# Performance work log

Hardware: AMD Instinct MI355X
Metric: run time of the kernel (lower is better)

## Reference

```python
import jax, jax.numpy as jnp
import numpy as np

N_NODES = 100000
N_EDGES = 1600000
IN_C, HID_C, OUT_C = 64, 64, 40


def setup_inputs() -> dict:
    key = jax.random.key(0)
    ks = jax.random.split(key, 8)
    x = jax.random.normal(ks[0], (N_NODES, IN_C), dtype=jnp.float32)
    edge_index = jax.random.randint(ks[1], (2, N_EDGES), 0, N_NODES, dtype=jnp.int32)
    s = 1.0 / np.sqrt(HID_C)
    W1 = jax.random.uniform(ks[2], (IN_C, HID_C), jnp.float32, -s, s)
    b1 = jnp.zeros((HID_C,), jnp.float32)
    Wh = jax.random.uniform(ks[3], (HID_C, HID_C), jnp.float32, -s, s)
    bh = jnp.zeros((HID_C,), jnp.float32)
    W2 = jax.random.uniform(ks[4], (HID_C, OUT_C), jnp.float32, -s, s)
    b2 = jnp.zeros((OUT_C,), jnp.float32)
    return {"x": x, "edge_index": edge_index, "W1": W1, "b1": b1,
            "Wh": Wh, "bh": bh, "W2": W2, "b2": b2}


def reference(x, edge_index, W1, b1, Wh, bh, W2, b2):
    N = x.shape[0]
    loop = jnp.arange(N, dtype=edge_index.dtype)
    # GCN normalization with self-loops: A_hat = D^-1/2 (A + I) D^-1/2
    src = jnp.concatenate([edge_index[0], loop])  # [E + N]
    dst = jnp.concatenate([edge_index[1], loop])
    deg = jax.ops.segment_sum(jnp.ones_like(dst, dtype=x.dtype), dst, num_segments=N)
    dinv = jnp.where(deg > 0, jax.lax.rsqrt(deg), 0.0)
    norm = dinv[src] * dinv[dst]  # [E + N]

    def gcn_conv(h, W, b):
        h = h @ W                              # [N, out]
        msg = h[src] * norm[:, None]           # gather + scale, [E+N, out]
        return jax.ops.segment_sum(msg, dst, num_segments=N) + b

    h = jax.nn.relu(gcn_conv(x, W1, b1))       # conv1 (dropout = identity in eval)
    h = jax.nn.relu(gcn_conv(h, Wh, bh))       # hidden_conv, layer_size=2 -> one pass
    h = gcn_conv(h, W2, b2)                    # conv2
    return jax.nn.log_softmax(h, axis=1)
```

## Files before the change

kernel.cpp:

```cpp
#include <hip/hip_runtime.h>
#include <hip/hip_bf16.h>
#include <math.h>

#define EPT 16
#define BCAP 16384

typedef _Float16 half8 __attribute__((ext_vector_type(8)));
typedef _Float16 half2v __attribute__((ext_vector_type(2)));
typedef float f32x4 __attribute__((ext_vector_type(4)));

__device__ __forceinline__ unsigned short f16r(float f) {
    _Float16 h = (_Float16)f;
    return __builtin_bit_cast(unsigned short, h);
}
__device__ __forceinline__ half2v h2(unsigned u) {
    return __builtin_bit_cast(half2v, u);
}


__global__ void scat1_kernel(const int* __restrict__ src, const int* __restrict__ dst,
                             int* __restrict__ cntg, unsigned* __restrict__ ebuf, int E) {
    __shared__ int lh[256];
    __shared__ int lbase[256];
    int tid = threadIdx.x;
    lh[tid] = 0;
    __syncthreads();
    int base = blockIdx.x * (256 * EPT);
    int ds[EPT], ss[EPT];
#pragma unroll
    for (int k = 0; k < EPT; ++k) {
        int e = base + k * 256 + tid;
        ds[k] = (e < E) ? dst[e] : -1;
        ss[k] = (e < E) ? src[e] : 0;
    }
#pragma unroll
    for (int k = 0; k < EPT; ++k) {
        if (ds[k] >= 0) atomicAdd(&lh[ds[k] >> 9], 1);
    }
    __syncthreads();
    if (lh[tid] > 0) lbase[tid] = atomicAdd(&cntg[tid], lh[tid]);
    lh[tid] = 0;
    __syncthreads();
#pragma unroll
    for (int k = 0; k < EPT; ++k) {
        if (ds[k] >= 0) {
            int b = ds[k] >> 9;
            int pos = lbase[b] + atomicAdd(&lh[b], 1);
            ebuf[(size_t)b * BCAP + pos] = ((unsigned)ss[k] << 9) | (unsigned)(ds[k] & 511);
        }
    }
}

__global__ void build_kernel(const unsigned* __restrict__ ebuf, const int* __restrict__ cntg,
                             int* __restrict__ row_ptr, int* __restrict__ col,
                             float* __restrict__ dinv, int N, int E) {
    __shared__ int deg[512];
    __shared__ int sh[256];
    int b = blockIdx.x;
    int tid = threadIdx.x;

    int v = cntg[tid];
    sh[tid] = v;
    __syncthreads();
    int val = v;
    for (int off = 1; off < 256; off <<= 1) {
        int add = 0;
        if (tid >= off) add = sh[tid - off];
        __syncthreads();
        val += add;
        sh[tid] = val;
        __syncthreads();
    }
    int start = (b > 0) ? sh[b - 1] : 0;
    int cnt = cntg[b];
    __syncthreads();

    int nodeBase = b << 9;
    int nn = N - nodeBase;
    if (nn > 512) nn = 512;
    if (nn < 0) nn = 0;
    const unsigned* eb = ebuf + (size_t)b * BCAP;

    deg[tid] = 0;
    deg[tid + 256] = 0;
    __syncthreads();
    for (int j = tid; j < cnt; j += 256) {
        atomicAdd(&deg[eb[j] & 511u], 1);
    }
    __syncthreads();

    int i0 = tid * 2, i1 = i0 + 1;
    int v0 = deg[i0], v1 = deg[i1];
    int tot = v0 + v1;
    sh[tid] = tot;
    __syncthreads();
    int val2 = tot;
    for (int off = 1; off < 256; off <<= 1) {
        int add = 0;
        if (tid >= off) add = sh[tid - off];
        __syncthreads();
        val2 += add;
        sh[tid] = val2;
        __syncthreads();
    }
    int excl = val2 - tot;

    if (i0 < nn) { row_ptr[nodeBase + i0] = start + excl;      dinv[nodeBase + i0] = rsqrtf((float)v0 + 1.0f); }
    if (i1 < nn) { row_ptr[nodeBase + i1] = start + excl + v0; dinv[nodeBase + i1] = rsqrtf((float)v1 + 1.0f); }
    if (b == 0 && tid == 0) row_ptr[N] = E;
    deg[i0] = start + excl;
    deg[i1] = start + excl + v0;
    __syncthreads();

    for (int j = tid; j < cnt; j += 256) {
        unsigned rec = eb[j];
        int pos = atomicAdd(&deg[rec & 511u], 1);
        col[pos] = (int)(rec >> 9);
    }
}


__global__ void cvtpack_kernel(const float* __restrict__ x, unsigned short* __restrict__ xb,
                               int n4, int npad, const float* __restrict__ dinv,
                               const float* __restrict__ W1, const float* __restrict__ Wh,
                               const float* __restrict__ W2, unsigned short* __restrict__ wp1,
                               unsigned short* __restrict__ wph, unsigned short* __restrict__ wp2) {
    int bid = blockIdx.x;
    if (bid < 16) {
        int i = bid * 256 + threadIdx.x;
        int j = i & 7;
        int lane = (i >> 3) & 63;
        int hh = (i >> 9) & 1;
        int t = i >> 10;
        int k = hh * 32 + (lane >> 4) * 8 + j;
        int cc = t * 16 + (lane & 15);
        wp1[i] = f16r(W1[k * 64 + cc]);
        wph[i] = f16r(Wh[k * 64 + cc]);
        if (t < 3) wp2[i] = f16r(cc < 40 ? W2[k * 40 + cc] : 0.f);
    } else {
        if (bid == 16 && threadIdx.x < 8) {
            *(uint4*)(xb + (size_t)npad * 64 + threadIdx.x * 8) = make_uint4(0, 0, 0, 0);
        }
        int i = (bid - 16) * 256 + threadIdx.x;
        if (i < n4) {
            float dn = dinv[i >> 4];
            float4 v = *(const float4*)(x + (size_t)i * 4);
            ushort4 o;
            o.x = f16r(v.x * dn); o.y = f16r(v.y * dn);
            o.z = f16r(v.z * dn); o.w = f16r(v.w * dn);
            *(ushort4*)(xb + (size_t)i * 4) = o;
        }
    }
}


__launch_bounds__(256, 8)
__global__ void fused_relu_kernel(const unsigned short* __restrict__ h,
                                  const int* __restrict__ row_ptr,
                                  const int* __restrict__ col,
                                  const float* __restrict__ dinv,
                                  const unsigned short* __restrict__ wp,
                                  const float* __restrict__ bias,
                                  unsigned short* __restrict__ out,
                                  int n, int zrow) {
    __shared__ unsigned short tile[16][72];
    if (blockIdx.x == 0 && threadIdx.x < 8) {
        *(uint4*)(out + (size_t)zrow * 64 + threadIdx.x * 8) = make_uint4(0, 0, 0, 0);
    }
    int tid = threadIdx.x;
    int w = tid >> 6;
    int lane = tid & 63;
    int sub = lane >> 3;
    unsigned choff = (lane & 7) * 16u;
    int nodeBase = blockIdx.x * 16;

#pragma unroll 1
    for (int i = 0; i < 4; ++i) {
        int row = w * 4 + i;
        int node = nodeBase + row;
        half2v a0 = (half2v)0, a1 = (half2v)0, a2 = (half2v)0, a3 = (half2v)0;
        if (node < n) {
            int beg = row_ptr[node];
            int deg = row_ptr[node + 1] - beg;
            float di = dinv[node];
            int total = deg + 1;
            int base = 0;
            while (base < total) {
                int vi = base + lane;
                int idx = zrow;
                if (vi < deg) idx = col[beg + vi];
                else if (vi == deg) idx = node;
                int cnt = min(total - base, 64);
#pragma unroll
                for (int it = 0; it < 4; ++it) {
                    int c0 = it * 16;
                    if (c0 >= cnt) break;
                    int s0 = __shfl(idx, c0 + sub);
                    int s1 = __shfl(idx, c0 + 8 + sub);
                    uint4 u0 = *(const uint4*)((const char*)h + (((unsigned)s0 << 7) + choff));
                    uint4 u1 = *(const uint4*)((const char*)h + (((unsigned)s1 << 7) + choff));
                    a0 += h2(u0.x);  a1 += h2(u0.y);  a2 += h2(u0.z);  a3 += h2(u0.w);
                    a0 += h2(u1.x);  a1 += h2(u1.y);  a2 += h2(u1.z);  a3 += h2(u1.w);
                }
                base += cnt;
            }
#pragma unroll
            for (int off = 8; off <= 32; off <<= 1) {
                a0 += __builtin_bit_cast(half2v, __shfl_xor(__builtin_bit_cast(int, a0), off));
                a1 += __builtin_bit_cast(half2v, __shfl_xor(__builtin_bit_cast(int, a1), off));
                a2 += __builtin_bit_cast(half2v, __shfl_xor(__builtin_bit_cast(int, a2), off));
                a3 += __builtin_bit_cast(half2v, __shfl_xor(__builtin_bit_cast(int, a3), off));
            }
            if (sub == 0) {
                half2v dih = __builtin_bit_cast(half2v, __builtin_amdgcn_cvt_pkrtz(di, di));
                a0 *= dih; a1 *= dih; a2 *= dih; a3 *= dih;
                uint4 o;
                o.x = __builtin_bit_cast(unsigned, a0);
                o.y = __builtin_bit_cast(unsigned, a1);
                o.z = __builtin_bit_cast(unsigned, a2);
                o.w = __builtin_bit_cast(unsigned, a3);
                *(uint4*)((char*)&tile[row][0] + choff) = o;
            }
        } else if (sub == 0) {
            *(uint4*)((char*)&tile[row][0] + choff) = make_uint4(0, 0, 0, 0);
        }
    }
    __syncthreads();

    int q = lane >> 4, c = lane & 15;
    half8 bf0 = *(const half8*)(wp + w * 1024 + lane * 8);
    half8 bf1 = *(const half8*)(wp + w * 1024 + 512 + lane * 8);
    float bs = bias[w * 16 + c];
    half8 a0 = *(const half8*)&tile[c][q * 8];
    half8 a1 = *(const half8*)&tile[c][32 + q * 8];
    f32x4 z = {0.f, 0.f, 0.f, 0.f};
    z = __builtin_amdgcn_mfma_f32_16x16x32_f16(a0, bf0, z, 0, 0, 0);
    z = __builtin_amdgcn_mfma_f32_16x16x32_f16(a1, bf1, z, 0, 0, 0);
#pragma unroll
    for (int r = 0; r < 4; ++r) {
        int node = nodeBase + q * 4 + r;
        if (node < n) {
            float dn = dinv[node];
            out[(size_t)node * 64 + w * 16 + c] = f16r(fmaxf(z[r] + bs, 0.f) * dn);
        }
    }
}


__launch_bounds__(256, 8)
__global__ void fused_lsm_kernel(const unsigned short* __restrict__ h,
                                 const int* __restrict__ row_ptr,
                                 const int* __restrict__ col,
                                 const float* __restrict__ dinv,
                                 const unsigned short* __restrict__ wp,
                                 const float* __restrict__ bias,
                                 float* __restrict__ out,
                                 int n, int zrow) {
    __shared__ unsigned short tile[16][72];
    int tid = threadIdx.x;
    int w = tid >> 6;
    int lane = tid & 63;
    int sub = lane >> 3;
    unsigned choff = (lane & 7) * 16u;
    int nodeBase = blockIdx.x * 16;

#pragma unroll 1
    for (int i = 0; i < 4; ++i) {
        int row = w * 4 + i;
        int node = nodeBase + row;
        half2v a0 = (half2v)0, a1 = (half2v)0, a2 = (half2v)0, a3 = (half2v)0;
        if (node < n) {
            int beg = row_ptr[node];
            int deg = row_ptr[node + 1] - beg;
            float di = dinv[node];
            int total = deg + 1;
            int base = 0;
            while (base < total) {
                int vi = base + lane;
                int idx = zrow;
                if (vi < deg) idx = col[beg + vi];
                else if (vi == deg) idx = node;
                int cnt = min(total - base, 64);
#pragma unroll
                for (int it = 0; it < 4; ++it) {
                    int c0 = it * 16;
                    if (c0 >= cnt) break;
                    int s0 = __shfl(idx, c0 + sub);
                    int s1 = __shfl(idx, c0 + 8 + sub);
                    uint4 u0 = *(const uint4*)((const char*)h + (((unsigned)s0 << 7) + choff));
                    uint4 u1 = *(const uint4*)((const char*)h + (((unsigned)s1 << 7) + choff));
                    a0 += h2(u0.x);  a1 += h2(u0.y);  a2 += h2(u0.z);  a3 += h2(u0.w);
                    a0 += h2(u1.x);  a1 += h2(u1.y);  a2 += h2(u1.z);  a3 += h2(u1.w);
                }
                base += cnt;
            }
#pragma unroll
            for (int off = 8; off <= 32; off <<= 1) {
                a0 += __builtin_bit_cast(half2v, __shfl_xor(__builtin_bit_cast(int, a0), off));
                a1 += __builtin_bit_cast(half2v, __shfl_xor(__builtin_bit_cast(int, a1), off));
                a2 += __builtin_bit_cast(half2v, __shfl_xor(__builtin_bit_cast(int, a2), off));
                a3 += __builtin_bit_cast(half2v, __shfl_xor(__builtin_bit_cast(int, a3), off));
            }
            if (sub == 0) {
                half2v dih = __builtin_bit_cast(half2v, __builtin_amdgcn_cvt_pkrtz(di, di));
                a0 *= dih; a1 *= dih; a2 *= dih; a3 *= dih;
                uint4 o;
                o.x = __builtin_bit_cast(unsigned, a0);
                o.y = __builtin_bit_cast(unsigned, a1);
                o.z = __builtin_bit_cast(unsigned, a2);
                o.w = __builtin_bit_cast(unsigned, a3);
                *(uint4*)((char*)&tile[row][0] + choff) = o;
            }
        } else if (sub == 0) {
            *(uint4*)((char*)&tile[row][0] + choff) = make_uint4(0, 0, 0, 0);
        }
    }
    __syncthreads();
    if (w != 0) return;

    int q = lane >> 4, c = lane & 15;
    bool v2ok = (c < 8);

    half8 bfrag[3][2];
#pragma unroll
    for (int t = 0; t < 3; ++t)
#pragma unroll
        for (int hh = 0; hh < 2; ++hh)
            bfrag[t][hh] = *(const half8*)(wp + t * 1024 + hh * 512 + lane * 8);
    float bs[3];
    bs[0] = bias[c];
    bs[1] = bias[16 + c];
    bs[2] = v2ok ? bias[32 + c] : 0.f;

    half8 a0 = *(const half8*)&tile[c][q * 8];
    half8 a1 = *(const half8*)&tile[c][32 + q * 8];

    f32x4 acc[3];
#pragma unroll
    for (int t = 0; t < 3; ++t) {
        f32x4 z = {0.f, 0.f, 0.f, 0.f};
        z = __builtin_amdgcn_mfma_f32_16x16x32_f16(a0, bfrag[t][0], z, 0, 0, 0);
        z = __builtin_amdgcn_mfma_f32_16x16x32_f16(a1, bfrag[t][1], z, 0, 0, 0);
        acc[t] = z;
    }

#pragma unroll
    for (int r = 0; r < 4; ++r) {
        int node = nodeBase + q * 4 + r;
        if (node < n) {
            float v0 = acc[0][r] + bs[0];
            float v1 = acc[1][r] + bs[1];
            float v2 = v2ok ? (acc[2][r] + bs[2]) : -INFINITY;
            float m = fmaxf(fmaxf(v0, v1), v2);
#pragma unroll
            for (int off = 1; off <= 8; off <<= 1) m = fmaxf(m, __shfl_xor(m, off));
            float s = expf(v0 - m) + expf(v1 - m) + (v2ok ? expf(v2 - m) : 0.f);
#pragma unroll
            for (int off = 1; off <= 8; off <<= 1) s += __shfl_xor(s, off);
            float ls = m + logf(s);
            float* orow = out + (size_t)node * 40;
            orow[c] = v0 - ls;
            orow[16 + c] = v1 - ls;
            if (v2ok) orow[32 + c] = v2 - ls;
        }
    }
}


extern "C" void kernel_launch(void* const* d_in, const int* in_sizes, int n_in,
                              void* d_out, int out_size, void* d_ws, size_t ws_size,
                              hipStream_t stream) {
    const float* x  = (const float*)d_in[0];
    const int* ei   = (const int*)d_in[1];
    const float* W1 = (const float*)d_in[2];
    const float* b1 = (const float*)d_in[3];
    const float* Wh = (const float*)d_in[4];
    const float* bh = (const float*)d_in[5];
    const float* W2 = (const float*)d_in[6];
    const float* b2 = (const float*)d_in[7];
    float* out = (float*)d_out;

    const int N = in_sizes[0] / 64;
    const int E = in_sizes[1] / 2;
    const int nbuk = (N + 511) >> 9;
    const int nTiles = (N + 15) / 16;
    const int Npad = nTiles * 16;

    const int* srcp = ei;
    const int* dstp = ei + E;

    size_t off = 0;
    auto alloc = [&](size_t bytes) {
        size_t o = off;
        off = (off + bytes + 255) & ~(size_t)255;
        return o;
    };
    char* ws = (char*)d_ws;
    int*      cntg    = (int*)(ws + alloc(256 * 4));
    int*      row_ptr = (int*)(ws + alloc((size_t)(N + 1) * 4));
    float*    dinv    = (float*)(ws + alloc((size_t)N * 4));
    int*      col     = (int*)(ws + alloc((size_t)E * 4));
    unsigned* ebuf    = (unsigned*)(ws + alloc((size_t)nbuk * BCAP * 4));
    unsigned short* wp1  = (unsigned short*)(ws + alloc(4096 * 2));
    unsigned short* wph  = (unsigned short*)(ws + alloc(4096 * 2));
    unsigned short* wp2  = (unsigned short*)(ws + alloc(3072 * 2));
    unsigned short* xb   = (unsigned short*)(ws + alloc((size_t)(Npad + 1) * 64 * 2));
    unsigned short* gA   = (unsigned short*)(ws + alloc((size_t)(Npad + 1) * 64 * 2));
    unsigned short* gB   = (unsigned short*)(ws + alloc((size_t)(Npad + 1) * 64 * 2));
    (void)ws_size;

    hipMemsetAsync(cntg, 0, 256 * 4, stream);

    const int ebGrid = (E + 256 * EPT - 1) / (256 * EPT);
    scat1_kernel<<<ebGrid, 256, 0, stream>>>(srcp, dstp, cntg, ebuf, E);
    build_kernel<<<nbuk, 256, 0, stream>>>(ebuf, cntg, row_ptr, col, dinv, N, E);

    const int n4 = N * 16;
    cvtpack_kernel<<<16 + (n4 + 255) / 256, 256, 0, stream>>>(x, xb, n4, Npad, dinv,
                                                              W1, Wh, W2, wp1, wph, wp2);

    fused_relu_kernel<<<nTiles, 256, 0, stream>>>(xb, row_ptr, col, dinv, wp1, b1, gA, N, Npad);
    fused_relu_kernel<<<nTiles, 256, 0, stream>>>(gA, row_ptr, col, dinv, wph, bh, gB, N, Npad);
    fused_lsm_kernel<<<nTiles, 256, 0, stream>>>(gB, row_ptr, col, dinv, wp2, b2, out, N, Npad);
}
```

Measured before the change: 252.0 us.

## Aggregate four nodes per wavefront with 16-lane groups in fused GCN kernels

The neighbor-gather phase of both fused kernels now assigns one 16-lane group per node, so a wavefront handles its four destination rows concurrently rather than serially. Each group loops in 16-edge chunks up to the wave's maximum chunk count, using two interleaved half-precision accumulator sets to shorten dependency chains. The cross-lane reduction shrinks to one shuffle step. This targets underutilised lanes and serial latency for low-degree nodes, at the cost of intra-wave imbalance when the four node degrees differ.

```diff
diff --git a/kernel.cpp b/kernel.cpp
--- a/kernel.cpp
+++ b/kernel.cpp
@@ -170,60 +170,57 @@
     int tid = threadIdx.x;
     int w = tid >> 6;
     int lane = tid & 63;
-    int sub = lane >> 3;
-    unsigned choff = (lane & 7) * 16u;
+    int g = lane >> 4;
+    int li = lane & 15;
+    int sub = li >> 3;
+    unsigned choff = (li & 7) * 16u;
     int nodeBase = blockIdx.x * 16;
-
-#pragma unroll 1
-    for (int i = 0; i < 4; ++i) {
-        int row = w * 4 + i;
-        int node = nodeBase + row;
-        half2v a0 = (half2v)0, a1 = (half2v)0, a2 = (half2v)0, a3 = (half2v)0;
-        if (node < n) {
-            int beg = row_ptr[node];
-            int deg = row_ptr[node + 1] - beg;
-            float di = dinv[node];
-            int total = deg + 1;
-            int base = 0;
-            while (base < total) {
-                int vi = base + lane;
-                int idx = zrow;
-                if (vi < deg) idx = col[beg + vi];
-                else if (vi == deg) idx = node;
-                int cnt = min(total - base, 64);
-#pragma unroll
-                for (int it = 0; it < 4; ++it) {
-                    int c0 = it * 16;
-                    if (c0 >= cnt) break;
-                    int s0 = __shfl(idx, c0 + sub);
-                    int s1 = __shfl(idx, c0 + 8 + sub);
-                    uint4 u0 = *(const uint4*)((const char*)h + (((unsigned)s0 << 7) + choff));
-                    uint4 u1 = *(const uint4*)((const char*)h + (((unsigned)s1 << 7) + choff));
-                    a0 += h2(u0.x);  a1 += h2(u0.y);  a2 += h2(u0.z);  a3 += h2(u0.w);
-                    a0 += h2(u1.x);  a1 += h2(u1.y);  a2 += h2(u1.z);  a3 += h2(u1.w);
-                }
-                base += cnt;
-            }
-#pragma unroll
-            for (int off = 8; off <= 32; off <<= 1) {
-                a0 += __builtin_bit_cast(half2v, __shfl_xor(__builtin_bit_cast(int, a0), off));
-                a1 += __builtin_bit_cast(half2v, __shfl_xor(__builtin_bit_cast(int, a1), off));
-                a2 += __builtin_bit_cast(half2v, __shfl_xor(__builtin_bit_cast(int, a2), off));
-                a3 += __builtin_bit_cast(half2v, __shfl_xor(__builtin_bit_cast(int, a3), off));
-            }
-            if (sub == 0) {
-                half2v dih = __builtin_bit_cast(half2v, __builtin_amdgcn_cvt_pkrtz(di, di));
-                a0 *= dih; a1 *= dih; a2 *= dih; a3 *= dih;
-                uint4 o;
-                o.x = __builtin_bit_cast(unsigned, a0);
-                o.y = __builtin_bit_cast(unsigned, a1);
-                o.z = __builtin_bit_cast(unsigned, a2);
-                o.w = __builtin_bit_cast(unsigned, a3);
-                *(uint4*)((char*)&tile[row][0] + choff) = o;
-            }
-        } else if (sub == 0) {
-            *(uint4*)((char*)&tile[row][0] + choff) = make_uint4(0, 0, 0, 0);
-        }
+    int row = w * 4 + g;
+    int node = nodeBase + row;
+
+    int beg = 0, deg = -1;
+    float di = 0.f;
+    if (node < n) {
+        beg = row_ptr[node];
+        deg = row_ptr[node + 1] - beg;
+        di = dinv[node];
+    }
+    int total = deg + 1;
+    int nb = (total + 15) >> 4;
+    nb = max(nb, __shfl_xor(nb, 16));
+    nb = max(nb, __shfl_xor(nb, 32));
+
+    half2v a0 = (half2v)0, a1 = (half2v)0, a2 = (half2v)0, a3 = (half2v)0;
+    half2v c0 = (half2v)0, c1 = (half2v)0, c2 = (half2v)0, c3 = (half2v)0;
+
+    for (int b = 0; b < nb; ++b) {
+        int e0 = (b << 4) + li;
+        int idx = zrow;
+        if (e0 < deg) idx = col[beg + e0];
+        else if (e0 == deg) idx = node;
+#pragma unroll
+        for (int it = 0; it < 8; ++it) {
+            int s = __shfl(idx, (g << 4) + it * 2 + sub);
+            uint4 u = *(const uint4*)((const char*)h + (((unsigned)s << 7) + choff));
+            if (it & 1) { c0 += h2(u.x); c1 += h2(u.y); c2 += h2(u.z); c3 += h2(u.w); }
+            else        { a0 += h2(u.x); a1 += h2(u.y); a2 += h2(u.z); a3 += h2(u.w); }
+        }
+    }
+    a0 += c0; a1 += c1; a2 += c2; a3 += c3;
+    a0 += __builtin_bit_cast(half2v, __shfl_xor(__builtin_bit_cast(int, a0), 8));
+    a1 += __builtin_bit_cast(half2v, __shfl_xor(__builtin_bit_cast(int, a1), 8));
+    a2 += __builtin_bit_cast(half2v, __shfl_xor(__builtin_bit_cast(int, a2), 8));
+    a3 += __builtin_bit_cast(half2v, __shfl_xor(__builtin_bit_cast(int, a3), 8));
+
+    if (sub == 0) {
+        half2v dih = __builtin_bit_cast(half2v, __builtin_amdgcn_cvt_pkrtz(di, di));
+        a0 *= dih; a1 *= dih; a2 *= dih; a3 *= dih;
+        uint4 o;
+        o.x = __builtin_bit_cast(unsigned, a0);
+        o.y = __builtin_bit_cast(unsigned, a1);
+        o.z = __builtin_bit_cast(unsigned, a2);
+        o.w = __builtin_bit_cast(unsigned, a3);
+        *(uint4*)((char*)&tile[row][0] + choff) = o;
     }
     __syncthreads();
 
@@ -231,17 +228,17 @@
     half8 bf0 = *(const half8*)(wp + w * 1024 + lane * 8);
     half8 bf1 = *(const half8*)(wp + w * 1024 + 512 + lane * 8);
     float bs = bias[w * 16 + c];
-    half8 a0 = *(const half8*)&tile[c][q * 8];
-    half8 a1 = *(const half8*)&tile[c][32 + q * 8];
+    half8 fa0 = *(const half8*)&tile[c][q * 8];
+    half8 fa1 = *(const half8*)&tile[c][32 + q * 8];
     f32x4 z = {0.f, 0.f, 0.f, 0.f};
-    z = __builtin_amdgcn_mfma_f32_16x16x32_f16(a0, bf0, z, 0, 0, 0);
-    z = __builtin_amdgcn_mfma_f32_16x16x32_f16(a1, bf1, z, 0, 0, 0);
+    z = __builtin_amdgcn_mfma_f32_16x16x32_f16(fa0, bf0, z, 0, 0, 0);
+    z = __builtin_amdgcn_mfma_f32_16x16x32_f16(fa1, bf1, z, 0, 0, 0);
 #pragma unroll
     for (int r = 0; r < 4; ++r) {
-        int node = nodeBase + q * 4 + r;
-        if (node < n) {
-            float dn = dinv[node];
-            out[(size_t)node * 64 + w * 16 + c] = f16r(fmaxf(z[r] + bs, 0.f) * dn);
+        int nodeW = nodeBase + q * 4 + r;
+        if (nodeW < n) {
+            float dn = dinv[nodeW];
+            out[(size_t)nodeW * 64 + w * 16 + c] = f16r(fmaxf(z[r] + bs, 0.f) * dn);
         }
     }
 }
@@ -260,60 +257,57 @@
     int tid = threadIdx.x;
     int w = tid >> 6;
     int lane = tid & 63;
-    int sub = lane >> 3;
-    unsigned choff = (lane & 7) * 16u;
+    int g = lane >> 4;
+    int li = lane & 15;
+    int sub = li >> 3;
+    unsigned choff = (li & 7) * 16u;
     int nodeBase = blockIdx.x * 16;
-
-#pragma unroll 1
-    for (int i = 0; i < 4; ++i) {
-        int row = w * 4 + i;
-        int node = nodeBase + row;
-        half2v a0 = (half2v)0, a1 = (half2v)0, a2 = (half2v)0, a3 = (half2v)0;
-        if (node < n) {
-            int beg = row_ptr[node];
-            int deg = row_ptr[node + 1] - beg;
-            float di = dinv[node];
-            int total = deg + 1;
-            int base = 0;
-            while (base < total) {
-                int vi = base + lane;
-                int idx = zrow;
-                if (vi < deg) idx = col[beg + vi];
-                else if (vi == deg) idx = node;
-                int cnt = min(total - base, 64);
-#pragma unroll
-                for (int it = 0; it < 4; ++it) {
-                    int c0 = it * 16;
-                    if (c0 >= cnt) break;
-                    int s0 = __shfl(idx, c0 + sub);
-                    int s1 = __shfl(idx, c0 + 8 + sub);
-                    uint4 u0 = *(const uint4*)((const char*)h + (((unsigned)s0 << 7) + choff));
-                    uint4 u1 = *(const uint4*)((const char*)h + (((unsigned)s1 << 7) + choff));
-                    a0 += h2(u0.x);  a1 += h2(u0.y);  a2 += h2(u0.z);  a3 += h2(u0.w);
-                    a0 += h2(u1.x);  a1 += h2(u1.y);  a2 += h2(u1.z);  a3 += h2(u1.w);
-                }
-                base += cnt;
-            }
-#pragma unroll
-            for (int off = 8; off <= 32; off <<= 1) {
-                a0 += __builtin_bit_cast(half2v, __shfl_xor(__builtin_bit_cast(int, a0), off));
-                a1 += __builtin_bit_cast(half2v, __shfl_xor(__builtin_bit_cast(int, a1), off));
-                a2 += __builtin_bit_cast(half2v, __shfl_xor(__builtin_bit_cast(int, a2), off));
-                a3 += __builtin_bit_cast(half2v, __shfl_xor(__builtin_bit_cast(int, a3), off));
-            }
-            if (sub == 0) {
-                half2v dih = __builtin_bit_cast(half2v, __builtin_amdgcn_cvt_pkrtz(di, di));
-                a0 *= dih; a1 *= dih; a2 *= dih; a3 *= dih;
-                uint4 o;
-                o.x = __builtin_bit_cast(unsigned, a0);
-                o.y = __builtin_bit_cast(unsigned, a1);
-                o.z = __builtin_bit_cast(unsigned, a2);
-                o.w = __builtin_bit_cast(unsigned, a3);
-                *(uint4*)((char*)&tile[row][0] + choff) = o;
-            }
-        } else if (sub == 0) {
-            *(uint4*)((char*)&tile[row][0] + choff) = make_uint4(0, 0, 0, 0);
-        }
+    int row = w * 4 + g;
+    int node = nodeBase + row;
+
+    int beg = 0, deg = -1;
+    float di = 0.f;
+    if (node < n) {
+        beg = row_ptr[node];
+        deg = row_ptr[node + 1] - beg;
+        di = dinv[node];
+    }
+    int total = deg + 1;
+    int nb = (total + 15) >> 4;
+    nb = max(nb, __shfl_xor(nb, 16));
+    nb = max(nb, __shfl_xor(nb, 32));
+
+    half2v a0 = (half2v)0, a1 = (half2v)0, a2 = (half2v)0, a3 = (half2v)0;
+    half2v c0a = (half2v)0, c1a = (half2v)0, c2a = (half2v)0, c3a = (half2v)0;
+
+    for (int b = 0; b < nb; ++b) {
+        int e0 = (b << 4) + li;
+        int idx = zrow;
+        if (e0 < deg) idx = col[beg + e0];
+        else if (e0 == deg) idx = node;
+#pragma unroll
+        for (int it = 0; it < 8; ++it) {
+            int s = __shfl(idx, (g << 4) + it * 2 + sub);
+            uint4 u = *(const uint4*)((const char*)h + (((unsigned)s << 7) + choff));
+            if (it & 1) { c0a += h2(u.x); c1a += h2(u.y); c2a += h2(u.z); c3a += h2(u.w); }
+            else        { a0 += h2(u.x);  a1 += h2(u.y);  a2 += h2(u.z);  a3 += h2(u.w); }
+        }
+    }
+    a0 += c0a; a1 += c1a; a2 += c2a; a3 += c3a;
+    a0 += __builtin_bit_cast(half2v, __shfl_xor(__builtin_bit_cast(int, a0), 8));
+    a1 += __builtin_bit_cast(half2v, __shfl_xor(__builtin_bit_cast(int, a1), 8));
+    a2 += __builtin_bit_cast(half2v, __shfl_xor(__builtin_bit_cast(int, a2), 8));
+    a3 += __builtin_bit_cast(half2v, __shfl_xor(__builtin_bit_cast(int, a3), 8));
+
+    if (sub == 0) {
+        half2v dih = __builtin_bit_cast(half2v, __builtin_amdgcn_cvt_pkrtz(di, di));
+        a0 *= dih; a1 *= dih; a2 *= dih; a3 *= dih;
+        uint4 o;
+        o.x = __builtin_bit_cast(unsigned, a0);
+        o.y = __builtin_bit_cast(unsigned, a1);
+        o.z = __builtin_bit_cast(unsigned, a2);
+        o.w = __builtin_bit_cast(unsigned, a3);
+        *(uint4*)((char*)&tile[row][0] + choff) = o;
     }
     __syncthreads();
     if (w != 0) return;
@@ -332,22 +326,22 @@
     bs[1] = bias[16 + c];
     bs[2] = v2ok ? bias[32 + c] : 0.f;
 
-    half8 a0 = *(const half8*)&tile[c][q * 8];
-    half8 a1 = *(const half8*)&tile[c][32 + q * 8];
+    half8 fa0 = *(const half8*)&tile[c][q * 8];
+    half8 fa1 = *(const half8*)&tile[c][32 + q * 8];
 
     f32x4 acc[3];
 #pragma unroll
     for (int t = 0; t < 3; ++t) {
         f32x4 z = {0.f, 0.f, 0.f, 0.f};
-        z = __builtin_amdgcn_mfma_f32_16x16x32_f16(a0, bfrag[t][0], z, 0, 0, 0);
-        z = __builtin_amdgcn_mfma_f32_16x16x32_f16(a1, bfrag[t][1], z, 0, 0, 0);
+        z = __builtin_amdgcn_mfma_f32_16x16x32_f16(fa0, bfrag[t][0], z, 0, 0, 0);
+        z = __builtin_amdgcn_mfma_f32_16x16x32_f16(fa1, bfrag[t][1], z, 0, 0, 0);
         acc[t] = z;
     }
 
 #pragma unroll
     for (int r = 0; r < 4; ++r) {
-        int node = nodeBase + q * 4 + r;
-        if (node < n) {
+        int nodeW = nodeBase + q * 4 + r;
+        if (nodeW < n) {
             float v0 = acc[0][r] + bs[0];
             float v1 = acc[1][r] + bs[1];
             float v2 = v2ok ? (acc[2][r] + bs[2]) : -INFINITY;
@@ -358,7 +352,7 @@
 #pragma unroll
             for (int off = 1; off <= 8; off <<= 1) s += __shfl_xor(s, off);
             float ls = m + logf(s);
-            float* orow = out + (size_t)node * 40;
+            float* orow = out + (size_t)nodeW * 40;
             orow[c] = v0 - ls;
             orow[16 + c] = v1 - ls;
             if (v2ok) orow[32 + c] = v2 - ls;
```

Result: faster. 229.0 us (-9.1%).
